# Optimization experiments

Hardware: AMD Instinct MI355X
Metric: run time of the kernel (lower is better)

The kernel has to match this reference:

```python
import jax, jax.numpy as jnp
import numpy as np

B, S, H = 2, 2048, 2560
NH, NKV, D = 8, 4, 256
SW = 1024
EPS = 1e-6
NEG = -1e9


def _rms(x, w=None, eps=EPS):
    y = x * jax.lax.rsqrt(jnp.mean(x * x, axis=-1, keepdims=True) + eps)
    return y * (1.0 + w) if w is not None else y


def _rope(x, cos, sin):
    # x: [B, h, S, D]; cos/sin: [1, 1, S, D] with duplicated half-frequencies
    half = x.shape[-1] // 2
    out = x * cos
    o1 = out[..., :half] - x[..., half:] * sin[..., :half]
    o2 = out[..., half:] + x[..., :half] * sin[..., half:]
    return jnp.concatenate([o1, o2], axis=-1)


def setup_inputs() -> dict:
    key = jax.random.key(0)
    ks = jax.random.split(key, 6)
    hidden_states = jax.random.normal(ks[0], (B, S, H), dtype=jnp.float32)
    Wq = jax.random.normal(ks[1], (NH * D, H), dtype=jnp.float32) * 0.02
    Wk = jax.random.normal(ks[2], (NKV * D, H), dtype=jnp.float32) * 0.02
    Wv = jax.random.normal(ks[3], (NKV * D, H), dtype=jnp.float32) * 0.02
    Wo = jax.random.normal(ks[4], (H, NH * D), dtype=jnp.float32) * 0.02
    q_norm_w = jnp.zeros((D,), dtype=jnp.float32)
    k_norm_w = jnp.zeros((D,), dtype=jnp.float32)
    # RoPE tables (standard theta=10000, duplicated halves as in torch ref)
    pos = jnp.arange(S, dtype=jnp.float32)
    inv = 1.0 / (10000.0 ** (jnp.arange(0, D, 2, dtype=jnp.float32) / D))
    freqs = pos[:, None] * inv[None, :]            # [S, D/2]
    emb = jnp.concatenate([freqs, freqs], axis=-1)  # [S, D]
    cos = jnp.cos(emb)[None, None]                 # [1,1,S,D]
    sin = jnp.sin(emb)[None, None]
    # causal + sliding-window additive mask (allowed: i-SW < j <= i)
    i = jnp.arange(S)[:, None]
    j = jnp.arange(S)[None, :]
    allowed = (j <= i) & (j > i - SW)
    attention_mask = jnp.where(allowed, 0.0, NEG).astype(jnp.float32)[None, None]
    return {"hidden_states": hidden_states, "attention_mask": attention_mask,
            "cos": cos, "sin": sin, "Wq": Wq, "Wk": Wk, "Wv": Wv, "Wo": Wo,
            "q_norm_w": q_norm_w, "k_norm_w": k_norm_w}


def reference(hidden_states, attention_mask, cos, sin, Wq, Wk, Wv, Wo, q_norm_w, k_norm_w):
    b, s, _ = hidden_states.shape
    xq = (hidden_states @ Wq.T).reshape(b, s, NH, D).transpose(0, 2, 1, 3)  # [B,NH,S,D]
    xq = _rms(xq, q_norm_w)
    xk = (hidden_states @ Wk.T).reshape(b, s, NKV, D)
    xv = (hidden_states @ Wv.T).reshape(b, s, NKV, D)
    xk = _rms(xk, k_norm_w)
    xv = _rms(xv)  # parameterless rms_norm on v
    xk = xk.transpose(0, 2, 1, 3)  # [B,NKV,S,D]
    xv = xv.transpose(0, 2, 1, 3)
    xq = _rope(xq, cos, sin)
    xk = _rope(xk, cos, sin)
    # expand_kv path: S >= sliding_window and NH != NKV -> repeat_interleave
    g = NH // NKV
    xk = jnp.repeat(xk, g, axis=1)
    xv = jnp.repeat(xv, g, axis=1)
    # scale=1.0 in original (no 1/sqrt(d))
    scores = jnp.einsum('bhqd,bhkd->bhqk', xq, xk) + attention_mask
    attn = jax.nn.softmax(scores, axis=-1)
    out = jnp.einsum('bhqk,bhkd->bhqd', attn, xv)
    out = out.transpose(0, 2, 1, 3).reshape(b, s, NH * D)
    return out @ Wo.T
```

## Files before the change

kernel.cpp:

```cpp
#include <hip/hip_runtime.h>

#define B_   2
#define S_   2048
#define H_   2560
#define NH_  8
#define NKV_ 4
#define D_   256
#define SW_  1024

#define QKV_LD 4096

typedef __attribute__((ext_vector_type(8))) short    short8;
typedef __attribute__((ext_vector_type(8))) _Float16 half8;
typedef __attribute__((ext_vector_type(4))) _Float16 half4;
typedef __attribute__((ext_vector_type(4))) float    floatx4;
typedef __attribute__((ext_vector_type(2))) float    floatx2;

typedef unsigned int __attribute__((address_space(1))) as1_uint;
typedef unsigned int __attribute__((address_space(3))) as3_uint;

static __device__ __forceinline__ void async16(const void* g, void* l) {
    __builtin_amdgcn_global_load_lds((const as1_uint*)g, (as3_uint*)l, 16, 0, 0);
}

__global__ __launch_bounds__(256) void conv_all(
    const float* __restrict__ s0, const float* __restrict__ s1,
    const float* __restrict__ s2, const float* __restrict__ s3,
    const float* __restrict__ s4,
    _Float16* __restrict__ d0, _Float16* __restrict__ d1,
    _Float16* __restrict__ d2, _Float16* __restrict__ d3,
    _Float16* __restrict__ d4)
{
    const float* src; _Float16* dst; int n4;
    switch (blockIdx.y) {
        case 0:  src = s0; dst = d0; n4 = 4096 * 2560 / 4; break;
        case 1:  src = s1; dst = d1; n4 = 2048 * 2560 / 4; break;
        case 2:  src = s2; dst = d2; n4 = 1024 * 2560 / 4; break;
        case 3:  src = s3; dst = d3; n4 = 1024 * 2560 / 4; break;
        default: src = s4; dst = d4; n4 = 2560 * 2048 / 4; break;
    }
    for (int i = blockIdx.x * 256 + threadIdx.x; i < n4; i += gridDim.x * 256) {
        floatx4 v = *(const floatx4*)(src + (size_t)i * 4);
        half4 h = { (_Float16)v.x, (_Float16)v.y, (_Float16)v.z, (_Float16)v.w };
        *(half4*)(dst + (size_t)i * 4) = h;
    }
}

template <int C_FP32>
__global__ __launch_bounds__(512, 2) void gemm256(
    const _Float16* __restrict__ A,
    const _Float16* __restrict__ Bm,
    void* __restrict__ Cv,
    int M, int N, int K, int NBX)
{
    (void)M;
    __shared__ __align__(16) _Float16 As[2][256 * 64];
    __shared__ __align__(16) _Float16 Bs[2][256 * 64];

    const int tid  = threadIdx.x;
    const int lane = tid & 63, w = tid >> 6;
    const int wr = w >> 2, wc = w & 3;
    const int quad = lane >> 4, l16 = lane & 15;

    const int nwg = gridDim.x, cpx = nwg >> 3;
    const int swz = (blockIdx.x & 7) * cpx + (blockIdx.x >> 3);
    const int mBase = (swz / NBX) * 256, nBase = (swz % NBX) * 256;

    const int NT = K >> 6;

    const int stRow = w * 8 + (lane >> 3);
    const int stCol = (((lane & 7) ^ (lane >> 3)) << 3);
    const int rdsw  = (l16 & 7) << 3;

    const _Float16* Ag = A  + (size_t)mBase * K;
    const _Float16* Bg = Bm + (size_t)nBase * K;

    floatx4 acc[8][4];
    const floatx4 fz = {0.f, 0.f, 0.f, 0.f};
#pragma unroll
    for (int i = 0; i < 8; ++i)
#pragma unroll
        for (int j = 0; j < 4; ++j) acc[i][j] = fz;

    auto stA = [&](int tt, int h, _Float16* dst) {
#pragma unroll
        for (int r = 0; r < 2; ++r) {
            const int rb = h * 128 + r * 64;
            async16(Ag + (size_t)(rb + stRow) * K + tt * 64 + stCol,
                    dst + (size_t)(rb + w * 8) * 64);
        }
    };
    auto stB = [&](int tt, int h, _Float16* dst) {
#pragma unroll
        for (int r = 0; r < 2; ++r) {
            const int rb = h * 128 + r * 64;
            async16(Bg + (size_t)(rb + stRow) * K + tt * 64 + stCol,
                    dst + (size_t)(rb + w * 8) * 64);
        }
    };

    stA(0, 0, &As[0][0]); stA(0, 1, &As[0][0]);
    stB(0, 0, &Bs[0][0]); stB(0, 1, &Bs[0][0]);
    if (NT > 1) { stB(1, 0, &Bs[1][0]); stB(1, 1, &Bs[1][0]); }
    asm volatile("s_waitcnt vmcnt(4)" ::: "memory");
    __builtin_amdgcn_s_barrier();

    auto tile = [&](int t, _Float16* Ab, _Float16* Bb, _Float16* Ao) {
        half8 bf[4][2], af[2][2];
#pragma unroll
        for (int c = 0; c < 4; ++c) {
            const int brow = wc * 64 + c * 16 + l16;
#pragma unroll
            for (int s = 0; s < 2; ++s)
                bf[c][s] = *(const half8*)&Bb[(size_t)brow * 64 + ((s * 32 + quad * 8) ^ rdsw)];
        }
#pragma unroll
        for (int r = 0; r < 2; ++r) {
            const int arow = wr * 128 + r * 16 + l16;
#pragma unroll
            for (int s = 0; s < 2; ++s)
                af[r][s] = *(const half8*)&Ab[(size_t)arow * 64 + ((s * 32 + quad * 8) ^ rdsw)];
        }
        if (t + 1 < NT) stA(t + 1, 0, Ao);
        asm volatile("s_waitcnt lgkmcnt(8)");
        __builtin_amdgcn_s_barrier();
        asm volatile("s_waitcnt lgkmcnt(0)");
        __builtin_amdgcn_s_setprio(1);
#pragma unroll
        for (int s = 0; s < 2; ++s)
#pragma unroll
            for (int c = 0; c < 4; ++c) {
                acc[0][c] = __builtin_amdgcn_mfma_f32_16x16x32_f16(af[0][s], bf[c][s], acc[0][c], 0, 0, 0);
                acc[1][c] = __builtin_amdgcn_mfma_f32_16x16x32_f16(af[1][s], bf[c][s], acc[1][c], 0, 0, 0);
            }
        __builtin_amdgcn_s_setprio(0);
        __builtin_amdgcn_s_barrier();
#pragma unroll
        for (int p = 1; p < 4; ++p) {
#pragma unroll
            for (int r = 0; r < 2; ++r) {
                const int arow = wr * 128 + (2 * p + r) * 16 + l16;
#pragma unroll
                for (int s = 0; s < 2; ++s)
                    af[r][s] = *(const half8*)&Ab[(size_t)arow * 64 + ((s * 32 + quad * 8) ^ rdsw)];
            }
            if (p == 1)      { if (t + 1 < NT) stA(t + 1, 1, Ao); }
            else if (p == 2) { if (t + 2 < NT) stB(t + 2, 0, Bb); }
            else             { if (t + 2 < NT) stB(t + 2, 1, Bb); }
            __builtin_amdgcn_s_barrier();
            asm volatile("s_waitcnt lgkmcnt(0)");
            __builtin_amdgcn_s_setprio(1);
#pragma unroll
            for (int s = 0; s < 2; ++s)
#pragma unroll
                for (int c = 0; c < 4; ++c) {
                    acc[2 * p][c]     = __builtin_amdgcn_mfma_f32_16x16x32_f16(af[0][s], bf[c][s], acc[2 * p][c], 0, 0, 0);
                    acc[2 * p + 1][c] = __builtin_amdgcn_mfma_f32_16x16x32_f16(af[1][s], bf[c][s], acc[2 * p + 1][c], 0, 0, 0);
                }
            __builtin_amdgcn_s_setprio(0);
            if (p == 3) {
                if (t < NT - 2) asm volatile("s_waitcnt vmcnt(4)" ::: "memory");
                else            asm volatile("s_waitcnt vmcnt(0)" ::: "memory");
            }
            __builtin_amdgcn_s_barrier();
        }
    };

    for (int t = 0; t < NT; t += 2) {
        tile(t,     &As[0][0], &Bs[0][0], &As[1][0]);
        tile(t + 1, &As[1][0], &Bs[1][0], &As[0][0]);
    }

#pragma unroll
    for (int fr = 0; fr < 8; ++fr) {
        const int row0 = mBase + wr * 128 + fr * 16 + quad * 4;
#pragma unroll
        for (int c = 0; c < 4; ++c) {
            const int col = nBase + wc * 64 + c * 16 + l16;
#pragma unroll
            for (int r = 0; r < 4; ++r) {
                const size_t idx = (size_t)(row0 + r) * N + col;
                if (C_FP32) ((float*)Cv)[idx] = acc[fr][c][r];
                else        ((_Float16*)Cv)[idx] = (_Float16)acc[fr][c][r];
            }
        }
    }
}

__global__ __launch_bounds__(256) void rmsrope_inplace(
    _Float16* __restrict__ qkv,
    const float* __restrict__ cosT,
    const float* __restrict__ sinT,
    const float* __restrict__ qw,
    const float* __restrict__ kw)
{
    const int t = blockIdx.x;
    const int s = t & (S_ - 1);
    const int tid = threadIdx.x, lane = tid & 63, w = tid >> 6;
    _Float16* row = qkv + (size_t)t * QKV_LD;
    const int d0 = lane * 2, d1 = 128 + lane * 2;

    floatx2 c0 = *(const floatx2*)(cosT + (size_t)s * D_ + d0);
    floatx2 c1 = *(const floatx2*)(cosT + (size_t)s * D_ + d1);
    floatx2 s0 = *(const floatx2*)(sinT + (size_t)s * D_ + d0);
    floatx2 s1 = *(const floatx2*)(sinT + (size_t)s * D_ + d1);
    floatx2 qw0 = *(const floatx2*)(qw + d0), qw1 = *(const floatx2*)(qw + d1);
    floatx2 kw0 = *(const floatx2*)(kw + d0), kw1 = *(const floatx2*)(kw + d1);

#pragma unroll
    for (int p = 0; p < 4; ++p) {
        const int v = w + p * 4;
        _Float16* x = row + v * D_;
        float x0a = (float)x[d0], x0b = (float)x[d0 + 1];
        float x1a = (float)x[d1], x1b = (float)x[d1 + 1];
        float ss = x0a * x0a + x0b * x0b + x1a * x1a + x1b * x1b;
#pragma unroll
        for (int off = 32; off > 0; off >>= 1) ss += __shfl_xor(ss, off, 64);
        const float rinv = rsqrtf(ss * (1.0f / 256.0f) + 1e-6f);
        if (v < 8) {
            const float y0a = x0a * rinv * (1.f + qw0.x), y0b = x0b * rinv * (1.f + qw0.y);
            const float y1a = x1a * rinv * (1.f + qw1.x), y1b = x1b * rinv * (1.f + qw1.y);
            x[d0] = (_Float16)(y0a * c0.x - y1a * s0.x);
            x[d0 + 1] = (_Float16)(y0b * c0.y - y1b * s0.y);
            x[d1] = (_Float16)(y1a * c1.x + y0a * s1.x);
            x[d1 + 1] = (_Float16)(y1b * c1.y + y0b * s1.y);
        } else if (v < 12) {
            const float y0a = x0a * rinv * (1.f + kw0.x), y0b = x0b * rinv * (1.f + kw0.y);
            const float y1a = x1a * rinv * (1.f + kw1.x), y1b = x1b * rinv * (1.f + kw1.y);
            x[d0] = (_Float16)(y0a * c0.x - y1a * s0.x);
            x[d0 + 1] = (_Float16)(y0b * c0.y - y1b * s0.y);
            x[d1] = (_Float16)(y1a * c1.x + y0a * s1.x);
            x[d1 + 1] = (_Float16)(y1b * c1.y + y0b * s1.y);
        } else {
            x[d0] = (_Float16)(x0a * rinv);
            x[d0 + 1] = (_Float16)(x0b * rinv);
            x[d1] = (_Float16)(x1a * rinv);
            x[d1 + 1] = (_Float16)(x1b * rinv);
        }
    }
}

__global__ __launch_bounds__(256) void transpose_v(
    const _Float16* __restrict__ qkv, _Float16* __restrict__ Vt)
{
    __shared__ _Float16 tile[64][66];
    const int s0 = blockIdx.x * 64;
    const int dd0 = blockIdx.y * 64;
    const int bk = blockIdx.z;
    const int b = bk >> 2, kvh = bk & 3;
    const _Float16* src = qkv + (size_t)(b * S_) * QKV_LD + 3072 + kvh * D_;
    _Float16* dst = Vt + (size_t)bk * D_ * S_;
    const int tx = threadIdx.x & 63, ty = threadIdx.x >> 6;
    for (int r = ty; r < 64; r += 4)
        tile[r][tx] = src[(size_t)(s0 + r) * QKV_LD + dd0 + tx];
    __syncthreads();
    for (int r = ty; r < 64; r += 4)
        dst[(size_t)(dd0 + r) * S_ + s0 + tx] = tile[tx][r];
}

#define KVB_ 64
#define PS_STRIDE 72

__global__ __launch_bounds__(256, 1) void attn_kernel(
    const _Float16* __restrict__ qkv,
    const _Float16* __restrict__ Vt,
    _Float16* __restrict__ Oa)
{
    __shared__ __align__(16) _Float16 Ks[2][KVB_ * 256];
    __shared__ __align__(16) _Float16 Vs[2][256 * KVB_];
    __shared__ __align__(16) _Float16 Ps[4][32 * PS_STRIDE];

    const int idx = blockIdx.x;
    const int swz = (idx & 7) * 32 + (idx >> 3);
    const int qt = swz & 15, h = (swz >> 4) & 7, b = swz >> 7;
    const int qb = qt * 128;
    const int kvh = h >> 1;

    const int tid = threadIdx.x, lane = tid & 63, w = tid >> 6;
    const int quad = lane >> 4, l16 = lane & 15;
    const int q0 = qb + w * 32;

    half8 qf[2][8];
#pragma unroll
    for (int mi = 0; mi < 2; ++mi) {
        const _Float16* Qrow = qkv + ((size_t)(b * S_ + q0 + mi * 16 + l16)) * QKV_LD + h * D_;
#pragma unroll
        for (int kst = 0; kst < 8; ++kst)
            qf[mi][kst] = *(const half8*)(Qrow + kst * 32 + quad * 8);
    }

    floatx4 o[2][16];
    const floatx4 fzero = {0.f, 0.f, 0.f, 0.f};
#pragma unroll
    for (int mi = 0; mi < 2; ++mi)
#pragma unroll
        for (int dt = 0; dt < 16; ++dt) o[mi][dt] = fzero;
    float mrow[2][4], lrow[2][4];
#pragma unroll
    for (int mi = 0; mi < 2; ++mi)
#pragma unroll
        for (int r = 0; r < 4; ++r) { mrow[mi][r] = -50000.f; lrow[mi][r] = 0.f; }

    const _Float16* Kbase  = qkv + (size_t)(b * S_) * QKV_LD + 2048 + kvh * D_;
    const _Float16* Vtbase = Vt + (size_t)(b * NKV_ + kvh) * D_ * S_;
    const int kb_start = (qb >= SW_) ? qb - SW_ : 0;
    const int kb_end = qb + 64;

    auto stage = [&](int kb, int bufi) {
#pragma unroll
        for (int p = 0; p < 8; ++p) {
            const int keyl = w * 16 + p * 2 + (lane >> 5);
            const int g = ((lane & 31) - keyl) & 31;
            async16(Kbase + (size_t)(kb + keyl) * QKV_LD + g * 8,
                    &Ks[bufi][(w * 16 + p * 2) * 256]);
        }
#pragma unroll
        for (int p = 0; p < 8; ++p) {
            const int drow = w * 64 + p * 8 + (lane >> 3);
            const int sc = (lane & 7) ^ ((lane >> 3) & 7);
            async16(Vtbase + (size_t)drow * S_ + kb + sc * 8,
                    &Vs[bufi][(w * 64 + p * 8) * KVB_]);
        }
    };

    int buf = 0;
    stage(kb_start, 0);

    for (int kb = kb_start; kb <= kb_end; kb += KVB_) {
        __syncthreads();
        if (kb + KVB_ <= kb_end) stage(kb + KVB_, buf ^ 1);

        if ((kb <= q0 + 31) && (kb + KVB_ - 1 >= q0 - (SW_ - 1))) {
            floatx4 sacc[4][2];
#pragma unroll
            for (int jt = 0; jt < 4; ++jt) { sacc[jt][0] = fzero; sacc[jt][1] = fzero; }
            __builtin_amdgcn_s_setprio(1);
#pragma unroll
            for (int jt = 0; jt < 4; ++jt) {
                const int keyl = jt * 16 + l16;
#pragma unroll
                for (int kst = 0; kst < 8; ++kst) {
                    const int crot = (kst * 4 + quad + keyl) & 31;
                    half8 kf = *(const half8*)&Ks[buf][keyl * 256 + crot * 8];
                    sacc[jt][0] = __builtin_amdgcn_mfma_f32_16x16x32_f16(qf[0][kst], kf, sacc[jt][0], 0, 0, 0);
                    sacc[jt][1] = __builtin_amdgcn_mfma_f32_16x16x32_f16(qf[1][kst], kf, sacc[jt][1], 0, 0, 0);
                }
            }
            __builtin_amdgcn_s_setprio(0);

            float sval[4][2][4], tmax[2][4];
#pragma unroll
            for (int mi = 0; mi < 2; ++mi)
#pragma unroll
                for (int r = 0; r < 4; ++r) tmax[mi][r] = -1e30f;
#pragma unroll
            for (int jt = 0; jt < 4; ++jt) {
                const int kg = kb + jt * 16 + l16;
#pragma unroll
                for (int mi = 0; mi < 2; ++mi)
#pragma unroll
                    for (int r = 0; r < 4; ++r) {
                        const int qg = q0 + mi * 16 + quad * 4 + r;
                        const bool ok = (unsigned)(qg - kg) < (unsigned)SW_;
                        const float vv = ok ? sacc[jt][mi][r] : -1e30f;
                        sval[jt][mi][r] = vv;
                        tmax[mi][r] = fmaxf(tmax[mi][r], vv);
                    }
            }
            float alpha[2][4];
            bool need = false;
#pragma unroll
            for (int mi = 0; mi < 2; ++mi)
#pragma unroll
                for (int r = 0; r < 4; ++r) {
                    float t = tmax[mi][r];
#pragma unroll
                    for (int off = 1; off < 16; off <<= 1)
                        t = fmaxf(t, __shfl_xor(t, off, 64));
                    const float mold = mrow[mi][r];
                    const float mnew = (t > mold + 8.f) ? t : mold;
                    alpha[mi][r] = __expf(mold - mnew);
                    need |= (mnew != mold);
                    mrow[mi][r] = mnew;
                    lrow[mi][r] *= alpha[mi][r];
                }
            if (__any(need)) {
#pragma unroll
                for (int mi = 0; mi < 2; ++mi)
#pragma unroll
                    for (int dt = 0; dt < 16; ++dt)
#pragma unroll
                        for (int r = 0; r < 4; ++r) o[mi][dt][r] *= alpha[mi][r];
            }
            float rsum[2][4] = {{0.f, 0.f, 0.f, 0.f}, {0.f, 0.f, 0.f, 0.f}};
#pragma unroll
            for (int jt = 0; jt < 4; ++jt)
#pragma unroll
                for (int mi = 0; mi < 2; ++mi)
#pragma unroll
                    for (int r = 0; r < 4; ++r) {
                        const float pv = __expf(sval[jt][mi][r] - mrow[mi][r]);
                        rsum[mi][r] += pv;
                        Ps[w][(mi * 16 + quad * 4 + r) * PS_STRIDE + jt * 16 + l16] = (_Float16)pv;
                    }
#pragma unroll
            for (int mi = 0; mi < 2; ++mi)
#pragma unroll
                for (int r = 0; r < 4; ++r) {
                    float s = rsum[mi][r];
#pragma unroll
                    for (int off = 1; off < 16; off <<= 1)
                        s += __shfl_xor(s, off, 64);
                    lrow[mi][r] += s;
                }

            __builtin_amdgcn_s_setprio(1);
#pragma unroll
            for (int ks = 0; ks < 2; ++ks) {
                half8 pa0 = *(const half8*)&Ps[w][(l16) * PS_STRIDE + ks * 32 + quad * 8];
                half8 pa1 = *(const half8*)&Ps[w][(16 + l16) * PS_STRIDE + ks * 32 + quad * 8];
#pragma unroll
                for (int dt = 0; dt < 16; ++dt) {
                    const int row = dt * 16 + l16;
                    half8 vf = *(const half8*)&Vs[buf][row * KVB_ + (((ks * 4 + quad) ^ (l16 & 7)) * 8)];
                    o[0][dt] = __builtin_amdgcn_mfma_f32_16x16x32_f16(pa0, vf, o[0][dt], 0, 0, 0);
                    o[1][dt] = __builtin_amdgcn_mfma_f32_16x16x32_f16(pa1, vf, o[1][dt], 0, 0, 0);
                }
            }
            __builtin_amdgcn_s_setprio(0);
        }
        buf ^= 1;
    }

#pragma unroll
    for (int mi = 0; mi < 2; ++mi)
#pragma unroll
        for (int r = 0; r < 4; ++r) {
            const int qrow = q0 + mi * 16 + quad * 4 + r;
            const float inv = (lrow[mi][r] > 0.f) ? (1.0f / lrow[mi][r]) : 0.f;
            _Float16* orow = Oa + ((size_t)(b * S_ + qrow)) * (NH_ * D_) + h * D_;
#pragma unroll
            for (int dt = 0; dt < 16; ++dt)
                orow[dt * 16 + l16] = (_Float16)(o[mi][dt][r] * inv);
        }
}

extern "C" void kernel_launch(void* const* d_in, const int* in_sizes, int n_in,
                              void* d_out, int out_size, void* d_ws, size_t ws_size,
                              hipStream_t stream)
{
    (void)in_sizes; (void)n_in; (void)out_size; (void)ws_size;
    const float* hid  = (const float*)d_in[0];
    const float* cosT = (const float*)d_in[2];
    const float* sinT = (const float*)d_in[3];
    const float* Wq   = (const float*)d_in[4];
    const float* Wk   = (const float*)d_in[5];
    const float* Wv   = (const float*)d_in[6];
    const float* Wo   = (const float*)d_in[7];
    const float* qw   = (const float*)d_in[8];
    const float* kw   = (const float*)d_in[9];
    float* out = (float*)d_out;

    char* ws = (char*)d_ws;
    _Float16* qkv  = (_Float16*)(ws);
    _Float16* attn = (_Float16*)(ws + 33554432ull);
    _Float16* hidH = (_Float16*)(ws + 50331648ull);
    _Float16* wQKV = (_Float16*)(ws + 71303168ull);
    _Float16* woH  = (_Float16*)(ws + 92274688ull);
    _Float16* Vt   = (_Float16*)(ws + 102760448ull);

    conv_all<<<dim3(512, 5), 256, 0, stream>>>(
        hid, Wq, Wk, Wv, Wo,
        hidH, wQKV, wQKV + (size_t)2048 * 2560, wQKV + (size_t)3072 * 2560, woH);

    gemm256<0><<<dim3(256), 512, 0, stream>>>(hidH, wQKV, qkv, 4096, 4096, 2560, 16);
    rmsrope_inplace<<<4096, 256, 0, stream>>>(qkv, cosT, sinT, qw, kw);
    transpose_v<<<dim3(32, 4, 8), 256, 0, stream>>>(qkv, Vt);
    attn_kernel<<<dim3(256), 256, 0, stream>>>(qkv, Vt, attn);
    gemm256<1><<<dim3(160), 512, 0, stream>>>(attn, woH, out, 4096, 2560, 2048, 10);
}
```

Baseline: 422.8 us.

## Split attention KV tiles across paired waves and merge partial softmax results

Doubles the attention block to 8 waves, with each pair of waves sharing a 32-row query slice and each wave handling half of every 64-key tile. The two partial (m, l, O) states are merged at the end through LDS reused from the K/V buffers. The goal is more waves per CU for latency hiding and a shorter per-wave serial chain on only 256 blocks. The cost is an extra LDS round trip plus a merge step, and launch_bounds(512,2) may raise register pressure on the large o accumulator. kb_start is also aligned to 64 so tiles sit on key boundaries.

```diff
diff --git a/kernel.cpp b/kernel.cpp
--- a/kernel.cpp
+++ b/kernel.cpp
@@ -259,16 +259,16 @@
 }
 
 #define KVB_ 64
-#define PS_STRIDE 72
-
-__global__ __launch_bounds__(256, 1) void attn_kernel(
+#define PS_STRIDE 36
+
+__global__ __launch_bounds__(512, 2) void attn_kernel(
     const _Float16* __restrict__ qkv,
     const _Float16* __restrict__ Vt,
     _Float16* __restrict__ Oa)
 {
     __shared__ __align__(16) _Float16 Ks[2][KVB_ * 256];
     __shared__ __align__(16) _Float16 Vs[2][256 * KVB_];
-    __shared__ __align__(16) _Float16 Ps[4][32 * PS_STRIDE];
+    __shared__ __align__(16) _Float16 Ps[8][32 * PS_STRIDE];
 
     const int idx = blockIdx.x;
     const int swz = (idx & 7) * 32 + (idx >> 3);
@@ -277,8 +277,10 @@
     const int kvh = h >> 1;
 
     const int tid = threadIdx.x, lane = tid & 63, w = tid >> 6;
+    const int qsub = w >> 1, kh = w & 1;
     const int quad = lane >> 4, l16 = lane & 15;
-    const int q0 = qb + w * 32;
+    const int q0 = qb + qsub * 32;
+    const int k0off = kh * 32;
 
     half8 qf[2][8];
 #pragma unroll
@@ -303,41 +305,42 @@
 
     const _Float16* Kbase  = qkv + (size_t)(b * S_) * QKV_LD + 2048 + kvh * D_;
     const _Float16* Vtbase = Vt + (size_t)(b * NKV_ + kvh) * D_ * S_;
-    const int kb_start = (qb >= SW_) ? qb - SW_ : 0;
-    const int kb_end = qb + 64;
+    const int kb_start = (qb >= SW_) ? (((qb - SW_ + 1) >> 6) << 6) : 0;
+    const int kb_last  = qb + 64;
 
     auto stage = [&](int kb, int bufi) {
 #pragma unroll
-        for (int p = 0; p < 8; ++p) {
-            const int keyl = w * 16 + p * 2 + (lane >> 5);
+        for (int p = 0; p < 4; ++p) {
+            const int keyl = w * 8 + p * 2 + (lane >> 5);
             const int g = ((lane & 31) - keyl) & 31;
             async16(Kbase + (size_t)(kb + keyl) * QKV_LD + g * 8,
-                    &Ks[bufi][(w * 16 + p * 2) * 256]);
-        }
-#pragma unroll
-        for (int p = 0; p < 8; ++p) {
-            const int drow = w * 64 + p * 8 + (lane >> 3);
+                    &Ks[bufi][(w * 8 + p * 2) * 256]);
+        }
+#pragma unroll
+        for (int p = 0; p < 4; ++p) {
+            const int drow = w * 32 + p * 8 + (lane >> 3);
             const int sc = (lane & 7) ^ ((lane >> 3) & 7);
             async16(Vtbase + (size_t)drow * S_ + kb + sc * 8,
-                    &Vs[bufi][(w * 64 + p * 8) * KVB_]);
+                    &Vs[bufi][(w * 32 + p * 8) * KVB_]);
         }
     };
 
     int buf = 0;
     stage(kb_start, 0);
 
-    for (int kb = kb_start; kb <= kb_end; kb += KVB_) {
+    for (int kb = kb_start; kb <= kb_last; kb += KVB_) {
         __syncthreads();
-        if (kb + KVB_ <= kb_end) stage(kb + KVB_, buf ^ 1);
-
-        if ((kb <= q0 + 31) && (kb + KVB_ - 1 >= q0 - (SW_ - 1))) {
-            floatx4 sacc[4][2];
-#pragma unroll
-            for (int jt = 0; jt < 4; ++jt) { sacc[jt][0] = fzero; sacc[jt][1] = fzero; }
+        if (kb + KVB_ <= kb_last) stage(kb + KVB_, buf ^ 1);
+
+        const int kw0 = kb + k0off;
+        if ((kw0 <= q0 + 31) && (kw0 + 31 >= q0 - (SW_ - 1))) {
+            floatx4 sacc[2][2];
+#pragma unroll
+            for (int jt = 0; jt < 2; ++jt) { sacc[jt][0] = fzero; sacc[jt][1] = fzero; }
             __builtin_amdgcn_s_setprio(1);
 #pragma unroll
-            for (int jt = 0; jt < 4; ++jt) {
-                const int keyl = jt * 16 + l16;
+            for (int jt = 0; jt < 2; ++jt) {
+                const int keyl = k0off + jt * 16 + l16;
 #pragma unroll
                 for (int kst = 0; kst < 8; ++kst) {
                     const int crot = (kst * 4 + quad + keyl) & 31;
@@ -348,14 +351,14 @@
             }
             __builtin_amdgcn_s_setprio(0);
 
-            float sval[4][2][4], tmax[2][4];
+            float sval[2][2][4], tmax[2][4];
 #pragma unroll
             for (int mi = 0; mi < 2; ++mi)
 #pragma unroll
                 for (int r = 0; r < 4; ++r) tmax[mi][r] = -1e30f;
 #pragma unroll
-            for (int jt = 0; jt < 4; ++jt) {
-                const int kg = kb + jt * 16 + l16;
+            for (int jt = 0; jt < 2; ++jt) {
+                const int kg = kw0 + jt * 16 + l16;
 #pragma unroll
                 for (int mi = 0; mi < 2; ++mi)
 #pragma unroll
@@ -394,7 +397,7 @@
             }
             float rsum[2][4] = {{0.f, 0.f, 0.f, 0.f}, {0.f, 0.f, 0.f, 0.f}};
 #pragma unroll
-            for (int jt = 0; jt < 4; ++jt)
+            for (int jt = 0; jt < 2; ++jt)
 #pragma unroll
                 for (int mi = 0; mi < 2; ++mi)
 #pragma unroll
@@ -415,14 +418,13 @@
                 }
 
             __builtin_amdgcn_s_setprio(1);
-#pragma unroll
-            for (int ks = 0; ks < 2; ++ks) {
-                half8 pa0 = *(const half8*)&Ps[w][(l16) * PS_STRIDE + ks * 32 + quad * 8];
-                half8 pa1 = *(const half8*)&Ps[w][(16 + l16) * PS_STRIDE + ks * 32 + quad * 8];
+            {
+                half8 pa0 = *(const half8*)&Ps[w][(l16) * PS_STRIDE + quad * 8];
+                half8 pa1 = *(const half8*)&Ps[w][(16 + l16) * PS_STRIDE + quad * 8];
 #pragma unroll
                 for (int dt = 0; dt < 16; ++dt) {
                     const int row = dt * 16 + l16;
-                    half8 vf = *(const half8*)&Vs[buf][row * KVB_ + (((ks * 4 + quad) ^ (l16 & 7)) * 8)];
+                    half8 vf = *(const half8*)&Vs[buf][row * KVB_ + ((((kh * 4 + quad)) ^ (l16 & 7)) * 8)];
                     o[0][dt] = __builtin_amdgcn_mfma_f32_16x16x32_f16(pa0, vf, o[0][dt], 0, 0, 0);
                     o[1][dt] = __builtin_amdgcn_mfma_f32_16x16x32_f16(pa1, vf, o[1][dt], 0, 0, 0);
                 }
@@ -432,17 +434,45 @@
         buf ^= 1;
     }
 
-#pragma unroll
-    for (int mi = 0; mi < 2; ++mi)
-#pragma unroll
-        for (int r = 0; r < 4; ++r) {
-            const int qrow = q0 + mi * 16 + quad * 4 + r;
-            const float inv = (lrow[mi][r] > 0.f) ? (1.0f / lrow[mi][r]) : 0.f;
-            _Float16* orow = Oa + ((size_t)(b * S_ + qrow)) * (NH_ * D_) + h * D_;
-#pragma unroll
-            for (int dt = 0; dt < 16; ++dt)
-                orow[dt * 16 + l16] = (_Float16)(o[mi][dt][r] * inv);
-        }
+    __syncthreads();
+    float* O1buf = (qsub < 2) ? ((float*)&Ks[0][0] + qsub * 8192)
+                              : ((float*)&Vs[0][0] + (qsub - 2) * 8192);
+    float* mlbuf = (float*)&Ps[0][0] + qsub * 64;
+    if (kh == 1) {
+#pragma unroll
+        for (int mi = 0; mi < 2; ++mi)
+#pragma unroll
+            for (int r = 0; r < 4; ++r) {
+                const int row = mi * 16 + quad * 4 + r;
+                if (l16 == 0) { mlbuf[row] = mrow[mi][r]; mlbuf[32 + row] = lrow[mi][r]; }
+#pragma unroll
+                for (int dt = 0; dt < 16; ++dt)
+                    O1buf[row * 256 + dt * 16 + l16] = o[mi][dt][r];
+            }
+    }
+    __syncthreads();
+    if (kh == 0) {
+#pragma unroll
+        for (int mi = 0; mi < 2; ++mi)
+#pragma unroll
+            for (int r = 0; r < 4; ++r) {
+                const int row = mi * 16 + quad * 4 + r;
+                const float m1 = mlbuf[row], l1 = mlbuf[32 + row];
+                const float m0 = mrow[mi][r], l0 = lrow[mi][r];
+                const float mm = fmaxf(m0, m1);
+                const float a0 = __expf(m0 - mm), a1 = __expf(m1 - mm);
+                const float lsum = l0 * a0 + l1 * a1;
+                const float inv = (lsum > 0.f) ? (1.0f / lsum) : 0.f;
+                const int qrow = q0 + row;
+                _Float16* orow = Oa + ((size_t)(b * S_ + qrow)) * (NH_ * D_) + h * D_;
+#pragma unroll
+                for (int dt = 0; dt < 16; ++dt) {
+                    const float v = (o[mi][dt][r] * a0 +
+                                     O1buf[row * 256 + dt * 16 + l16] * a1) * inv;
+                    orow[dt * 16 + l16] = (_Float16)v;
+                }
+            }
+    }
 }
 
 extern "C" void kernel_launch(void* const* d_in, const int* in_sizes, int n_in,
@@ -476,6 +506,6 @@
     gemm256<0><<<dim3(256), 512, 0, stream>>>(hidH, wQKV, qkv, 4096, 4096, 2560, 16);
     rmsrope_inplace<<<4096, 256, 0, stream>>>(qkv, cosT, sinT, qw, kw);
     transpose_v<<<dim3(32, 4, 8), 256, 0, stream>>>(qkv, Vt);
-    attn_kernel<<<dim3(256), 256, 0, stream>>>(qkv, Vt, attn);
+    attn_kernel<<<dim3(256), 512, 0, stream>>>(qkv, Vt, attn);
     gemm256<1><<<dim3(160), 512, 0, stream>>>(attn, woH, out, 4096, 2560, 2048, 10);
 }
```

Result: slower. 522.0 us (+23.5%).
